# Kernel tuning notes

Hardware: AMD Instinct MI355X
Metric: run time of the kernel (lower is better)

The kernel has to match this reference:

```python
import jax
import jax.numpy as jnp
import numpy as np

N = 256   # hardcoded in the torch module via expand(256, 256)
D = 256
K = 16
M_MARGIN = 0.6
T_THRESH = 0.0025
EPS = 1e-12


def setup_inputs() -> dict:
    key = jax.random.key(0)
    k1, k2 = jax.random.split(key)
    yi = jax.random.normal(k1, (N, D), dtype=jnp.float32)
    yi_t = jax.random.normal(k2, (N, D), dtype=jnp.float32)
    return {"yi": yi, "yi_t": yi_t}


def _l2_normalize(x):
    return x / jnp.sqrt(jnp.sum(x * x, axis=-1, keepdims=True) + EPS)


def reference(yi, yi_t):
    yi_n = _l2_normalize(yi)      # [N, D]
    yit_n = _l2_normalize(yi_t)   # [N, D]

    # pairwise half-distances: [N, N]
    diff = yi_n[:, None, :] - yi_n[None, :, :]           # [N, N, D]
    dis_yii = 0.5 * jnp.sqrt(jnp.sum(diff * diff, axis=-1) + EPS)

    # K+1 smallest distances per row (self is smallest)
    neg_vals, topk_idx = jax.lax.top_k(-dis_yii, K + 1)  # [N, K+1]
    nbr_idx = topk_idx[:, 1:]                            # [N, K] exclude self

    yj = yi_n[nbr_idx]                                   # [N, K, D]
    dis_yij = 0.5 * jnp.sqrt(jnp.sum((yi_n[:, None, :] - yj) ** 2, axis=-1) + EPS)
    dis_yi_tj = 0.5 * jnp.sqrt(jnp.sum((yit_n[:, None, :] - yj) ** 2, axis=-1) + EPS)

    e1 = jnp.sum((dis_yij - dis_yi_tj) ** 2 - T_THRESH)

    # margin term: dist(yi, yi_t) + m - (second smallest pairwise dist)
    dis_yi_yi_t = 0.5 * jnp.sqrt(jnp.sum((yi_n - yit_n) ** 2, axis=-1) + EPS)  # [N]
    second_nn = -neg_vals[:, 1]                          # [N]
    out = dis_yi_yi_t + M_MARGIN - second_nn
    e2 = jnp.sum(jnp.maximum(out, 0.0))

    return e1 + e2
```

## Files before the change

kernel.cpp:

```cpp
#include <hip/hip_runtime.h>
#include <math.h>

#define NN 256
#define DD 256
#define KK 16
#define M_MARGIN 0.6f
#define T_THRESH 0.0025f
#define EPS 1e-12f

__global__ void __launch_bounds__(1024) blcd_row_kernel(
    const float* __restrict__ yi, const float* __restrict__ yit,
    float* __restrict__ partial)
{
    __shared__ float s_yi[DD];
    __shared__ float s_yit[DD];
    __shared__ float sdis[NN];
    __shared__ float red[16];

    const int i = blockIdx.x;
    const int t = threadIdx.x;
    const int j = t >> 2;
    const int s = t & 3;
    const int w = t >> 6;

    if (t < DD) {
        s_yi[t]  = yi [i * DD + t];
        s_yit[t] = yit[i * DD + t];
    }

    const float4* __restrict__ rj = (const float4*)(yi + j * DD);
    float4 p[16];
    #pragma unroll
    for (int k = 0; k < 16; ++k) p[k] = rj[4 * k + s];

    __syncthreads();

    const float4* __restrict__ si = (const float4*)s_yi;
    float4 q4  = make_float4(0.f, 0.f, 0.f, 0.f);
    float4 nn4 = make_float4(0.f, 0.f, 0.f, 0.f);
    float4 uu4 = make_float4(0.f, 0.f, 0.f, 0.f);
    #pragma unroll
    for (int k = 0; k < 16; ++k) {
        const float4 y = p[k];
        const float4 u = si[4 * k + s];
        q4.x  += y.x * u.x; q4.y  += y.y * u.y; q4.z  += y.z * u.z; q4.w  += y.w * u.w;
        nn4.x += y.x * y.x; nn4.y += y.y * y.y; nn4.z += y.z * y.z; nn4.w += y.w * y.w;
        uu4.x += u.x * u.x; uu4.y += u.y * u.y; uu4.z += u.z * u.z; uu4.w += u.w * u.w;
    }
    float q  = (q4.x  + q4.y ) + (q4.z  + q4.w );
    float nn = (nn4.x + nn4.y) + (nn4.z + nn4.w);
    float uu = (uu4.x + uu4.y) + (uu4.z + uu4.w);
    q  += __shfl_xor(q,  1, 64);  q  += __shfl_xor(q,  2, 64);
    nn += __shfl_xor(nn, 1, 64);  nn += __shfl_xor(nn, 2, 64);
    uu += __shfl_xor(uu, 1, 64);  uu += __shfl_xor(uu, 2, 64);

    const float inv_ni = 1.0f / sqrtf(uu + EPS);
    const float inv_nt = 1.0f / sqrtf(nn + EPS);
    const float c   = q * inv_nt * inv_ni;
    const float myv = 0.5f * sqrtf(fmaxf(2.0f - 2.0f * c, 0.0f) + EPS);
    if (s == 0) sdis[j] = myv;
    __syncthreads();

    int rank = 0;
    const float4* sd4 = (const float4*)sdis;
    #pragma unroll
    for (int m = 0; m < 16; ++m) {
        const int k = 4 * m + s;
        float4 v = sd4[k];
        const int jj = k * 4;
        rank += (v.x < myv || (v.x == myv && (jj + 0) < j)) ? 1 : 0;
        rank += (v.y < myv || (v.y == myv && (jj + 1) < j)) ? 1 : 0;
        rank += (v.z < myv || (v.z == myv && (jj + 2) < j)) ? 1 : 0;
        rank += (v.w < myv || (v.w == myv && (jj + 3) < j)) ? 1 : 0;
    }
    rank += __shfl_xor(rank, 1, 64);
    rank += __shfl_xor(rank, 2, 64);

    float contrib = 0.0f;
    if (rank >= 1 && rank <= KK) {
        const float4* __restrict__ sit = (const float4*)s_yit;
        float4 qt4 = make_float4(0.f, 0.f, 0.f, 0.f);
        float4 vv4 = make_float4(0.f, 0.f, 0.f, 0.f);
        float4 uv4 = make_float4(0.f, 0.f, 0.f, 0.f);
        #pragma unroll
        for (int k = 0; k < 16; ++k) {
            const float4 y = p[k];
            const float4 u = si [4 * k + s];
            const float4 v = sit[4 * k + s];
            qt4.x += y.x * v.x; qt4.y += y.y * v.y; qt4.z += y.z * v.z; qt4.w += y.w * v.w;
            vv4.x += v.x * v.x; vv4.y += v.y * v.y; vv4.z += v.z * v.z; vv4.w += v.w * v.w;
            uv4.x += u.x * v.x; uv4.y += u.y * v.y; uv4.z += u.z * v.z; uv4.w += u.w * v.w;
        }
        float qt = (qt4.x + qt4.y) + (qt4.z + qt4.w);
        float vv = (vv4.x + vv4.y) + (vv4.z + vv4.w);
        float uv = (uv4.x + uv4.y) + (uv4.z + uv4.w);
        qt += __shfl_xor(qt, 1, 64);  qt += __shfl_xor(qt, 2, 64);
        vv += __shfl_xor(vv, 1, 64);  vv += __shfl_xor(vv, 2, 64);
        uv += __shfl_xor(uv, 1, 64);  uv += __shfl_xor(uv, 2, 64);

        const float inv_nit = 1.0f / sqrtf(vv + EPS);
        const float ct   = qt * inv_nt * inv_nit;
        const float myvt = 0.5f * sqrtf(fmaxf(2.0f - 2.0f * ct, 0.0f) + EPS);
        if (s == 0) {
            const float dd = myv - myvt;
            contrib = dd * dd - T_THRESH;
            if (rank == 1) {
                const float cc = uv * inv_ni * inv_nit;
                const float d_iit = 0.5f * sqrtf(fmaxf(2.0f - 2.0f * cc, 0.0f) + EPS);
                contrib += fmaxf(d_iit + M_MARGIN - myv, 0.0f);
            }
        }
    }

    #pragma unroll
    for (int off = 32; off > 0; off >>= 1) contrib += __shfl_down(contrib, off, 64);
    if ((t & 63) == 0) red[w] = contrib;
    __syncthreads();
    if (t == 0) {
        float tot = ((red[0]  + red[1])  + (red[2]  + red[3]))
                  + ((red[4]  + red[5])  + (red[6]  + red[7]))
                  + ((red[8]  + red[9])  + (red[10] + red[11]))
                  + ((red[12] + red[13]) + (red[14] + red[15]));
        partial[i] = tot;
    }
}

__global__ void __launch_bounds__(64) blcd_reduce_kernel(
    const float* __restrict__ partial, float* __restrict__ out)
{
    const int t = threadIdx.x;
    const float4 v4 = ((const float4*)partial)[t];
    float v = (v4.x + v4.y) + (v4.z + v4.w);
    #pragma unroll
    for (int off = 32; off > 0; off >>= 1) v += __shfl_down(v, off, 64);
    if (t == 0) out[0] = v;
}

extern "C" void kernel_launch(void* const* d_in, const int* in_sizes, int n_in,
                              void* d_out, int out_size, void* d_ws, size_t ws_size,
                              hipStream_t stream) {
    (void)in_sizes; (void)n_in; (void)out_size; (void)ws_size;

    const float* yi  = (const float*)d_in[0];
    const float* yit = (const float*)d_in[1];
    float* out = (float*)d_out;
    float* ws  = (float*)d_ws;

    blcd_row_kernel<<<NN, 1024, 0, stream>>>(yi, yit, ws);
    blcd_reduce_kernel<<<1, 64, 0, stream>>>(ws, out);
}
```

Before: 64.55 us.

## Rank neighbors by cosine key and compact top-K work into one wave

```diff
diff --git a/kernel.cpp b/kernel.cpp
--- a/kernel.cpp
+++ b/kernel.cpp
@@ -14,18 +14,20 @@
 {
     __shared__ float s_yi[DD];
     __shared__ float s_yit[DD];
-    __shared__ float sdis[NN];
-    __shared__ float red[16];
+    __shared__ float skey[NN];
+    __shared__ int   nbrj [KK];
+    __shared__ float nbrq [KK];
+    __shared__ float nbrnn[KK];
 
     const int i = blockIdx.x;
     const int t = threadIdx.x;
     const int j = t >> 2;
     const int s = t & 3;
-    const int w = t >> 6;
 
+    float a = 0.0f, b = 0.0f;
     if (t < DD) {
-        s_yi[t]  = yi [i * DD + t];
-        s_yit[t] = yit[i * DD + t];
+        a = yi [i * DD + t];
+        b = yit[i * DD + t];
     }
 
     const float4* __restrict__ rj = (const float4*)(yi + j * DD);
@@ -33,96 +35,104 @@
     #pragma unroll
     for (int k = 0; k < 16; ++k) p[k] = rj[4 * k + s];
 
+    if (t < DD) { s_yi[t] = a; s_yit[t] = b; }
     __syncthreads();
 
     const float4* __restrict__ si = (const float4*)s_yi;
     float4 q4  = make_float4(0.f, 0.f, 0.f, 0.f);
     float4 nn4 = make_float4(0.f, 0.f, 0.f, 0.f);
-    float4 uu4 = make_float4(0.f, 0.f, 0.f, 0.f);
     #pragma unroll
     for (int k = 0; k < 16; ++k) {
         const float4 y = p[k];
         const float4 u = si[4 * k + s];
         q4.x  += y.x * u.x; q4.y  += y.y * u.y; q4.z  += y.z * u.z; q4.w  += y.w * u.w;
         nn4.x += y.x * y.x; nn4.y += y.y * y.y; nn4.z += y.z * y.z; nn4.w += y.w * y.w;
-        uu4.x += u.x * u.x; uu4.y += u.y * u.y; uu4.z += u.z * u.z; uu4.w += u.w * u.w;
     }
     float q  = (q4.x  + q4.y ) + (q4.z  + q4.w );
     float nn = (nn4.x + nn4.y) + (nn4.z + nn4.w);
-    float uu = (uu4.x + uu4.y) + (uu4.z + uu4.w);
     q  += __shfl_xor(q,  1, 64);  q  += __shfl_xor(q,  2, 64);
     nn += __shfl_xor(nn, 1, 64);  nn += __shfl_xor(nn, 2, 64);
-    uu += __shfl_xor(uu, 1, 64);  uu += __shfl_xor(uu, 2, 64);
 
-    const float inv_ni = 1.0f / sqrtf(uu + EPS);
-    const float inv_nt = 1.0f / sqrtf(nn + EPS);
-    const float c   = q * inv_nt * inv_ni;
-    const float myv = 0.5f * sqrtf(fmaxf(2.0f - 2.0f * c, 0.0f) + EPS);
-    if (s == 0) sdis[j] = myv;
+    const float key = q * (1.0f / sqrtf(nn + EPS));
+    if (s == 0) skey[j] = key;
     __syncthreads();
 
     int rank = 0;
-    const float4* sd4 = (const float4*)sdis;
+    const float4* sk4 = (const float4*)skey;
     #pragma unroll
     for (int m = 0; m < 16; ++m) {
         const int k = 4 * m + s;
-        float4 v = sd4[k];
+        float4 v = sk4[k];
         const int jj = k * 4;
-        rank += (v.x < myv || (v.x == myv && (jj + 0) < j)) ? 1 : 0;
-        rank += (v.y < myv || (v.y == myv && (jj + 1) < j)) ? 1 : 0;
-        rank += (v.z < myv || (v.z == myv && (jj + 2) < j)) ? 1 : 0;
-        rank += (v.w < myv || (v.w == myv && (jj + 3) < j)) ? 1 : 0;
+        rank += (v.x > key || (v.x == key && (jj + 0) < j)) ? 1 : 0;
+        rank += (v.y > key || (v.y == key && (jj + 1) < j)) ? 1 : 0;
+        rank += (v.z > key || (v.z == key && (jj + 2) < j)) ? 1 : 0;
+        rank += (v.w > key || (v.w == key && (jj + 3) < j)) ? 1 : 0;
     }
     rank += __shfl_xor(rank, 1, 64);
     rank += __shfl_xor(rank, 2, 64);
 
+    if (s == 0 && rank >= 1 && rank <= KK) {
+        nbrj [rank - 1] = j;
+        nbrq [rank - 1] = q;
+        nbrnn[rank - 1] = nn;
+    }
+    __syncthreads();
+
+    if (t >= 64) return;
+
+    const int g  = t >> 2;
+    const int s2 = t & 3;
+    const int   jn  = nbrj [g];
+    const float qn  = nbrq [g];
+    const float nnn = nbrnn[g];
+
+    const float4* __restrict__ rn  = (const float4*)(yi + jn * DD);
+    const float4* __restrict__ sit = (const float4*)s_yit;
+    float4 qt4 = make_float4(0.f, 0.f, 0.f, 0.f);
+    float4 vv4 = make_float4(0.f, 0.f, 0.f, 0.f);
+    float4 uv4 = make_float4(0.f, 0.f, 0.f, 0.f);
+    float4 uu4 = make_float4(0.f, 0.f, 0.f, 0.f);
+    #pragma unroll
+    for (int k = 0; k < 16; ++k) {
+        const float4 y = rn [4 * k + s2];
+        const float4 u = si [4 * k + s2];
+        const float4 v = sit[4 * k + s2];
+        qt4.x += y.x * v.x; qt4.y += y.y * v.y; qt4.z += y.z * v.z; qt4.w += y.w * v.w;
+        vv4.x += v.x * v.x; vv4.y += v.y * v.y; vv4.z += v.z * v.z; vv4.w += v.w * v.w;
+        uv4.x += u.x * v.x; uv4.y += u.y * v.y; uv4.z += u.z * v.z; uv4.w += u.w * v.w;
+        uu4.x += u.x * u.x; uu4.y += u.y * u.y; uu4.z += u.z * u.z; uu4.w += u.w * u.w;
+    }
+    float qt = (qt4.x + qt4.y) + (qt4.z + qt4.w);
+    float vv = (vv4.x + vv4.y) + (vv4.z + vv4.w);
+    float uv = (uv4.x + uv4.y) + (uv4.z + uv4.w);
+    float uu = (uu4.x + uu4.y) + (uu4.z + uu4.w);
+    qt += __shfl_xor(qt, 1, 64);  qt += __shfl_xor(qt, 2, 64);
+    vv += __shfl_xor(vv, 1, 64);  vv += __shfl_xor(vv, 2, 64);
+    uv += __shfl_xor(uv, 1, 64);  uv += __shfl_xor(uv, 2, 64);
+    uu += __shfl_xor(uu, 1, 64);  uu += __shfl_xor(uu, 2, 64);
+
+    const float inv_ni  = 1.0f / sqrtf(uu  + EPS);
+    const float inv_nit = 1.0f / sqrtf(vv  + EPS);
+    const float inv_nt  = 1.0f / sqrtf(nnn + EPS);
+    const float c    = qn * inv_nt * inv_ni;
+    const float ct   = qt * inv_nt * inv_nit;
+    const float myv  = 0.5f * sqrtf(fmaxf(2.0f - 2.0f * c , 0.0f) + EPS);
+    const float myvt = 0.5f * sqrtf(fmaxf(2.0f - 2.0f * ct, 0.0f) + EPS);
+
     float contrib = 0.0f;
-    if (rank >= 1 && rank <= KK) {
-        const float4* __restrict__ sit = (const float4*)s_yit;
-        float4 qt4 = make_float4(0.f, 0.f, 0.f, 0.f);
-        float4 vv4 = make_float4(0.f, 0.f, 0.f, 0.f);
-        float4 uv4 = make_float4(0.f, 0.f, 0.f, 0.f);
-        #pragma unroll
-        for (int k = 0; k < 16; ++k) {
-            const float4 y = p[k];
-            const float4 u = si [4 * k + s];
-            const float4 v = sit[4 * k + s];
-            qt4.x += y.x * v.x; qt4.y += y.y * v.y; qt4.z += y.z * v.z; qt4.w += y.w * v.w;
-            vv4.x += v.x * v.x; vv4.y += v.y * v.y; vv4.z += v.z * v.z; vv4.w += v.w * v.w;
-            uv4.x += u.x * v.x; uv4.y += u.y * v.y; uv4.z += u.z * v.z; uv4.w += u.w * v.w;
-        }
-        float qt = (qt4.x + qt4.y) + (qt4.z + qt4.w);
-        float vv = (vv4.x + vv4.y) + (vv4.z + vv4.w);
-        float uv = (uv4.x + uv4.y) + (uv4.z + uv4.w);
-        qt += __shfl_xor(qt, 1, 64);  qt += __shfl_xor(qt, 2, 64);
-        vv += __shfl_xor(vv, 1, 64);  vv += __shfl_xor(vv, 2, 64);
-        uv += __shfl_xor(uv, 1, 64);  uv += __shfl_xor(uv, 2, 64);
-
-        const float inv_nit = 1.0f / sqrtf(vv + EPS);
-        const float ct   = qt * inv_nt * inv_nit;
-        const float myvt = 0.5f * sqrtf(fmaxf(2.0f - 2.0f * ct, 0.0f) + EPS);
-        if (s == 0) {
-            const float dd = myv - myvt;
-            contrib = dd * dd - T_THRESH;
-            if (rank == 1) {
-                const float cc = uv * inv_ni * inv_nit;
-                const float d_iit = 0.5f * sqrtf(fmaxf(2.0f - 2.0f * cc, 0.0f) + EPS);
-                contrib += fmaxf(d_iit + M_MARGIN - myv, 0.0f);
-            }
+    if (s2 == 0) {
+        const float dd = myv - myvt;
+        contrib = dd * dd - T_THRESH;
+        if (g == 0) {
+            const float cc = uv * inv_ni * inv_nit;
+            const float d_iit = 0.5f * sqrtf(fmaxf(2.0f - 2.0f * cc, 0.0f) + EPS);
+            contrib += fmaxf(d_iit + M_MARGIN - myv, 0.0f);
         }
     }
-
     #pragma unroll
     for (int off = 32; off > 0; off >>= 1) contrib += __shfl_down(contrib, off, 64);
-    if ((t & 63) == 0) red[w] = contrib;
-    __syncthreads();
-    if (t == 0) {
-        float tot = ((red[0]  + red[1])  + (red[2]  + red[3]))
-                  + ((red[4]  + red[5])  + (red[6]  + red[7]))
-                  + ((red[8]  + red[9])  + (red[10] + red[11]))
-                  + ((red[12] + red[13]) + (red[14] + red[15]));
-        partial[i] = tot;
-    }
+    if (t == 0) partial[i] = contrib;
 }
 
 __global__ void __launch_bounds__(64) blcd_reduce_kernel(
```

After: 62.72 us. 2.8% less time.
